# Performance work log

Hardware: AMD Instinct MI355X
Metric: run time of the kernel (lower is better)

Reference implementation:

```python
import jax, jax.numpy as jnp
import numpy as np

# Sizes (must match input_specs)
N_CHR, E_CHR = 50000, 500000
N_SLV, E_SLV = 30000, 300000
B = 256            # number of graphs in the batch
FEAT = 64          # num_node_feats
DIM = 128          # hidden dim
HALF = DIM // 2    # last GCN layer output
ENS = 3            # ensemble per branch type


def setup_inputs() -> dict:
    key = jax.random.key(0)
    ks = jax.random.split(key, 20)
    g = lambda k, shape, fan_in: jax.random.normal(k, shape, dtype=jnp.float32) / np.sqrt(fan_in)
    inp = {
        'chr_x': jax.random.normal(ks[0], (N_CHR, FEAT), dtype=jnp.float32),
        'slv_x': jax.random.normal(ks[1], (N_SLV, FEAT), dtype=jnp.float32),
        'chr_edge_index': jax.random.randint(ks[2], (2, E_CHR), 0, N_CHR),
        'slv_edge_index': jax.random.randint(ks[3], (2, E_SLV), 0, N_SLV),
        'chr_x_batch': jnp.sort(jax.random.randint(ks[4], (N_CHR,), 0, B)),
        'slv_x_batch': jnp.sort(jax.random.randint(ks[5], (N_SLV,), 0, B)),
        # GCN weights, stacked over ensemble (GCNConv: bias=False)
        'chr_W0': g(ks[6], (ENS, FEAT, DIM), FEAT),
        'chr_W1': g(ks[7], (ENS, DIM, DIM), DIM),
        'chr_W2': g(ks[8], (ENS, DIM, HALF), DIM),
        'slv_W0': g(ks[9], (ENS, FEAT, DIM), FEAT),
        'slv_W1': g(ks[10], (ENS, DIM, DIM), DIM),
        'slv_W2': g(ks[11], (ENS, DIM, HALF), DIM),
        # per-ensemble projection heads (nn.Linear with bias)
        'cfc_W': g(ks[12], (ENS, HALF, DIM), HALF),
        'cfc_b': jnp.zeros((ENS, DIM), dtype=jnp.float32),
        'sfc_W': g(ks[13], (ENS, HALF, DIM), HALF),
        'sfc_b': jnp.zeros((ENS, DIM), dtype=jnp.float32),
        # final MLP head
        'fc1_W': g(ks[14], (2 * ENS * DIM, DIM), 2 * ENS * DIM),
        'fc1_b': jnp.zeros((DIM,), dtype=jnp.float32),
        'fc2_W': g(ks[15], (DIM, 1), DIM),
        'fc2_b': jnp.zeros((1,), dtype=jnp.float32),
    }
    return inp


def _gcn(x, W, src, dst, n_nodes):
    # GCNConv(normalize=False, bias=False, aggr='add'):
    # out[i] = sum_{(j,i) in E} (x @ W)[j]   (no self-loops, no normalization)
    h = x @ W
    return jax.ops.segment_sum(h[src], dst, num_segments=n_nodes)


def _branch(x, W0, W1, W2, edge_index, batch_ids, n_nodes):
    src, dst = edge_index[0], edge_index[1]
    h = jax.nn.relu(_gcn(x, W0, src, dst, n_nodes))
    h = jax.nn.relu(_gcn(h, W1, src, dst, n_nodes))
    h = jax.nn.relu(_gcn(h, W2, src, dst, n_nodes))
    # global_add_pool
    return jax.ops.segment_sum(h, batch_ids, num_segments=B)  # [B, HALF]


def reference(chr_x, slv_x, chr_W0, chr_W1, chr_W2, slv_W0, slv_W1, slv_W2,
              cfc_W, cfc_b, sfc_W, sfc_b, fc1_W, fc1_b, fc2_W, fc2_b,
              chr_edge_index, slv_edge_index, chr_x_batch, slv_x_batch):
    # vmap over the ensemble dimension (independent GCN stacks share inputs)
    rep_chr = jax.vmap(lambda w0, w1, w2: _branch(chr_x, w0, w1, w2, chr_edge_index, chr_x_batch, N_CHR))(
        chr_W0, chr_W1, chr_W2)  # [ENS, B, HALF]
    rep_slv = jax.vmap(lambda w0, w1, w2: _branch(slv_x, w0, w1, w2, slv_edge_index, slv_x_batch, N_SLV))(
        slv_W0, slv_W1, slv_W2)  # [ENS, B, HALF]
    ind_chr = jax.nn.relu(jnp.einsum('ebd,edh->ebh', rep_chr, cfc_W) + cfc_b[:, None, :])  # [ENS, B, DIM]
    ind_slv = jax.nn.relu(jnp.einsum('ebd,edh->ebh', rep_slv, sfc_W) + sfc_b[:, None, :])
    # torch.cat(ind_chr + ind_slv, dim=1): chr branches first, then slv branches
    hg = jnp.concatenate([
        jnp.transpose(ind_chr, (1, 0, 2)).reshape(B, ENS * DIM),
        jnp.transpose(ind_slv, (1, 0, 2)).reshape(B, ENS * DIM)], axis=1)  # [B, 2*ENS*DIM]
    hg = jax.nn.relu(hg @ fc1_W + fc1_b)
    out = hg @ fc2_W + fc2_b  # [B, 1]
    return out
```

## Files before the change

### kernel.cpp

```cpp
#include <hip/hip_runtime.h>

#define N_CHR 50000
#define E_CHR 500000
#define N_SLV 30000
#define E_SLV 300000
#define E_TOT (E_CHR + E_SLV)
#define BATCH_B 256
#define FEAT 64
#define DIM 128
#define HALF 64
#define ENSN 3
#define CB_CHR ((N_CHR + 255) / 256)
#define CB_SLV ((N_SLV + 255) / 256)
#define CB_TOT (CB_CHR + CB_SLV)
#define NBLK 128
#define CHUNK ((E_TOT + NBLK - 1) / NBLK)

typedef unsigned int u32;
typedef unsigned short u16;
typedef __attribute__((ext_vector_type(8))) short short8;
typedef __attribute__((ext_vector_type(4))) float floatx4;
typedef __attribute__((ext_vector_type(2))) unsigned int u32x2;


__device__ inline u16 f2b(float f) {
    u32 u = __builtin_bit_cast(u32, f);
    u += 0x7FFFu + ((u >> 16) & 1u);
    return (u16)(u >> 16);
}
__device__ inline float b2f_lo(u32 v) { return __builtin_bit_cast(float, v << 16); }
__device__ inline float b2f_hi(u32 v) { return __builtin_bit_cast(float, v & 0xFFFF0000u); }
__device__ inline u32 packb(float a, float b) { return (u32)f2b(a) | ((u32)f2b(b) << 16); }


__global__ void xconv_k(const float* __restrict__ xc, const float* __restrict__ xs,
                        u16* __restrict__ oc, u16* __restrict__ os) {
    const int nc = N_CHR * FEAT, ns = N_SLV * FEAT;
    int i = blockIdx.x * blockDim.x + threadIdx.x;
    int stride = gridDim.x * blockDim.x;
    for (; i < nc + ns; i += stride) {
        if (i < nc) oc[i] = f2b(xc[i]);
        else os[i - nc] = f2b(xs[i - nc]);
    }
}


__global__ void wconv_k(const float* __restrict__ Wc, const float* __restrict__ Ws,
                        u16* __restrict__ Wtc, u16* __restrict__ Wts, int K, int N) {
    const float* W = blockIdx.z ? Ws : Wc;
    u16* Wt = blockIdx.z ? Wts : Wtc;
    int e = blockIdx.y;
    int idx = blockIdx.x * 256 + threadIdx.x;
    if (idx >= K * N) return;
    int k = idx / N, nn = idx - k * N;
    Wt[((size_t)e * N + nn) * K + k] = f2b(W[(size_t)e * K * N + idx]);
}


__global__ __launch_bounds__(256) void hist_blocks_k(
        const int* __restrict__ cdst, const int* __restrict__ sdst,
        int* __restrict__ gh, int* __restrict__ btot) {
    __shared__ int h[CB_TOT];
    int blk = blockIdx.x, t = threadIdx.x;
    for (int i = t; i < CB_TOT; i += 256) h[i] = 0;
    __syncthreads();
    int s = blk * CHUNK, e = s + CHUNK;
    if (e > E_TOT) e = E_TOT;
    for (int i = s + t; i < e; i += 256) {
        int bkt = (i < E_CHR) ? (cdst[i] >> 8) : (CB_CHR + (sdst[i - E_CHR] >> 8));
        atomicAdd(&h[bkt], 1);
    }
    __syncthreads();
    for (int j = t; j < CB_TOT; j += 256) {
        gh[j * NBLK + blk] = h[j];
        if (h[j]) atomicAdd(&btot[j], h[j]);
    }
}

__global__ void coarse_scan_k(const int* __restrict__ cnt, int* __restrict__ off) {
    int t = threadIdx.x;
    const int PER = (CB_TOT + 63) / 64;
    int loc[PER];
    int sum = 0;
    int s = t * PER;
// ... 82 lines not shown
}

__global__ __launch_bounds__(256) void bucket_sort_k(
        const u32* __restrict__ staging, const int* __restrict__ coff,
        int* __restrict__ off_c, int* __restrict__ off_s,
        int* __restrict__ csr_c, int* __restrict__ csr_s) {
    int b = blockIdx.x, t = threadIdx.x;
    int isS = b >= CB_CHR;
    int base = coff[b], end = coff[b + 1];
    int n = isS ? N_SLV : N_CHR;
    int* off = isS ? off_s : off_c;
    int* csr = isS ? csr_s : csr_c;
    int outBase = isS ? base - E_CHR : base;
    int nodeBase = (isS ? (b - CB_CHR) : b) << 8;
    __shared__ int hist[256];
    __shared__ int cur[256];
    hist[t] = 0;
    __syncthreads();
    for (int i = base + t; i < end; i += 256)
        atomicAdd(&hist[staging[i] >> 17], 1);
    __syncthreads();
    int p = block_exscan(hist[t]);
    int node = nodeBase + t;
    if (node <= n) off[node] = outBase + p;
    cur[t] = p;
    __syncthreads();
    for (int i = base + t; i < end; i += 256) {
        u32 v = staging[i];
        int pos = atomicAdd(&cur[v >> 17], 1);
        csr[outBase + pos] = (int)(v & 0x1FFFFu);
    }
}

__global__ void bounds_both_k(const int* __restrict__ cb, const int* __restrict__ sb,
                              int* __restrict__ start_c, int* __restrict__ start_s) {
    int t = threadIdx.x + blockIdx.x * blockDim.x;
    int isS = t >= 320;
    int b = isS ? t - 320 : t;
    if (b > BATCH_B) return;
    const int* batch = isS ? sb : cb;
    int n = isS ? N_SLV : N_CHR;
    int* start = isS ? start_s : start_c;
    if (b == BATCH_B) { start[b] = n; return; }
    int lo = 0, hi = n;
    while (lo < hi) {
        int mid = (lo + hi) >> 1;
        if (batch[mid] < b) lo = mid + 1; else hi = mid;
    }
    start[b] = lo;
}


__global__ __launch_bounds__(256) void agg1_k(
        const u16* __restrict__ Xc, const int* __restrict__ offc, const int* __restrict__ csrc,
        u16* __restrict__ Yc, int nc,
        const u16* __restrict__ Xs, const int* __restrict__ offs, const int* __restrict__ csrs,
        u16* __restrict__ Ys, int ns) {
    int z = blockIdx.z;
    const u32* X32 = (const u32*)(z ? Xs : Xc);
    const int* off = z ? offs : offc;
    const int* csr = z ? csrs : csrc;
    u32* Y32 = (u32*)(z ? Ys : Yc);
    int n = z ? ns : nc;
    int i = blockIdx.x * 8 + (threadIdx.x >> 5);
    if (i >= n) return;
    int fp = threadIdx.x & 31;
    int s = off[i], e2 = off[i + 1];
    float a0 = 0.f, a1 = 0.f;
    int j = s;
    for (; j + 3 < e2; j += 4) {
        u32 v0 = X32[(size_t)csr[j] * 32 + fp];
        u32 v1 = X32[(size_t)csr[j + 1] * 32 + fp];
        u32 v2 = X32[(size_t)csr[j + 2] * 32 + fp];
        u32 v3 = X32[(size_t)csr[j + 3] * 32 + fp];
        a0 += b2f_lo(v0) + b2f_lo(v1) + b2f_lo(v2) + b2f_lo(v3);
        a1 += b2f_hi(v0) + b2f_hi(v1) + b2f_hi(v2) + b2f_hi(v3);
    }
    for (; j < e2; j++) {
        u32 v = X32[(size_t)csr[j] * 32 + fp];
        a0 += b2f_lo(v); a1 += b2f_hi(v);
    }
    Y32[(size_t)i * 32 + fp] = packb(a0, a1);
}


template<bool RELU>
__global__ __launch_bounds__(256) void aggb128_k(
        const u16* __restrict__ Hc, const int* __restrict__ offc, const int* __restrict__ csrc,
        u16* __restrict__ Yc, int nc,
        const u16* __restrict__ Hs, const int* __restrict__ offs, const int* __restrict__ csrs,
        u16* __restrict__ Ys, int ns) {
    int z = blockIdx.z, e = blockIdx.y;
    int n = z ? ns : nc;
    const int* off = z ? offs : offc;
    const int* csr = z ? csrs : csrc;
    const u32* He = (const u32*)((z ? Hs : Hc) + (size_t)e * n * DIM);
    u32* Ye = (u32*)((z ? Ys : Yc) + (size_t)e * n * DIM);
    int i = blockIdx.x * 8 + (threadIdx.x >> 5);
    if (i >= n) return;
    int fp = threadIdx.x & 31;
    int s = off[i], e2 = off[i + 1];
    float a0 = 0.f, a1 = 0.f, a2 = 0.f, a3 = 0.f;
    int j = s;
    for (; j + 3 < e2; j += 4) {
        u32x2 v0 = *(const u32x2*)(He + (size_t)csr[j] * 64 + fp * 2);
        u32x2 v1 = *(const u32x2*)(He + (size_t)csr[j + 1] * 64 + fp * 2);
        u32x2 v2 = *(const u32x2*)(He + (size_t)csr[j + 2] * 64 + fp * 2);
        u32x2 v3 = *(const u32x2*)(He + (size_t)csr[j + 3] * 64 + fp * 2);
        a0 += b2f_lo(v0.x) + b2f_lo(v1.x) + b2f_lo(v2.x) + b2f_lo(v3.x);
        a1 += b2f_hi(v0.x) + b2f_hi(v1.x) + b2f_hi(v2.x) + b2f_hi(v3.x);
        a2 += b2f_lo(v0.y) + b2f_lo(v1.y) + b2f_lo(v2.y) + b2f_lo(v3.y);
        a3 += b2f_hi(v0.y) + b2f_hi(v1.y) + b2f_hi(v2.y) + b2f_hi(v3.y);
    }
    for (; j < e2; j++) {
        u32x2 v = *(const u32x2*)(He + (size_t)csr[j] * 64 + fp * 2);
        a0 += b2f_lo(v.x); a1 += b2f_hi(v.x);
        a2 += b2f_lo(v.y); a3 += b2f_hi(v.y);
    }
    if (RELU) {
        a0 = fmaxf(a0, 0.f); a1 = fmaxf(a1, 0.f);
        a2 = fmaxf(a2, 0.f); a3 = fmaxf(a3, 0.f);
    }
    u32x2 o; o.x = packb(a0, a1); o.y = packb(a2, a3);
    *(u32x2*)(Ye + (size_t)i * 64 + fp * 2) = o;
}


template<bool RELU>
__global__ __launch_bounds__(256) void aggb64_k(
        const u16* __restrict__ Hc, const int* __restrict__ offc, const int* __restrict__ csrc,
        u16* __restrict__ Yc, int nc,
        const u16* __restrict__ Hs, const int* __restrict__ offs, const int* __restrict__ csrs,
        u16* __restrict__ Ys, int ns) {
    int z = blockIdx.z, e = blockIdx.y;
    int n = z ? ns : nc;
    const int* off = z ? offs : offc;
    const int* csr = z ? csrs : csrc;
    const u32* He = (const u32*)((z ? Hs : Hc) + (size_t)e * n * HALF);
    u32* Ye = (u32*)((z ? Ys : Yc) + (size_t)e * n * HALF);
    int i = blockIdx.x * 16 + (threadIdx.x >> 4);
    if (i >= n) return;
    int fp = threadIdx.x & 15;
    int s = off[i], e2 = off[i + 1];
    float a0 = 0.f, a1 = 0.f, a2 = 0.f, a3 = 0.f;
    int j = s;
    for (; j + 3 < e2; j += 4) {
        u32x2 v0 = *(const u32x2*)(He + (size_t)csr[j] * 32 + fp * 2);
        u32x2 v1 = *(const u32x2*)(He + (size_t)csr[j + 1] * 32 + fp * 2);
        u32x2 v2 = *(const u32x2*)(He + (size_t)csr[j + 2] * 32 + fp * 2);
        u32x2 v3 = *(const u32x2*)(He + (size_t)csr[j + 3] * 32 + fp * 2);
        a0 += b2f_lo(v0.x) + b2f_lo(v1.x) + b2f_lo(v2.x) + b2f_lo(v3.x);
        a1 += b2f_hi(v0.x) + b2f_hi(v1.x) + b2f_hi(v2.x) + b2f_hi(v3.x);
        a2 += b2f_lo(v0.y) + b2f_lo(v1.y) + b2f_lo(v2.y) + b2f_lo(v3.y);
        a3 += b2f_hi(v0.y) + b2f_hi(v1.y) + b2f_hi(v2.y) + b2f_hi(v3.y);
    }
    for (; j < e2; j++) {
        u32x2 v = *(const u32x2*)(He + (size_t)csr[j] * 32 + fp * 2);
        a0 += b2f_lo(v.x); a1 += b2f_hi(v.x);
        a2 += b2f_lo(v.y); a3 += b2f_hi(v.y);
    }
    if (RELU) {
        a0 = fmaxf(a0, 0.f); a1 = fmaxf(a1, 0.f);
        a2 = fmaxf(a2, 0.f); a3 = fmaxf(a3, 0.f);
    }
    u32x2 o; o.x = packb(a0, a1); o.y = packb(a2, a3);
    *(u32x2*)(Ye + (size_t)i * 32 + fp * 2) = o;
}


#define WPAD 8

template<int K, int COLS, bool RELU>
__global__ __launch_bounds__(256) void gemm_mfma_k(
        const u16* __restrict__ Xc, size_t esc, const u16* __restrict__ Wtc,
        u16* __restrict__ Yc, int nc,
        const u16* __restrict__ Xs, size_t ess, const u16* __restrict__ Wts,
        u16* __restrict__ Ys, int ns) {
    __shared__ u16 wlds[COLS * (K + WPAD)];
    const int z = blockIdx.z, e = blockIdx.y;
    const int n = z ? ns : nc;
    const u16* Xe = (z ? Xs : Xc) + (size_t)e * (z ? ess : esc);
    const u16* We = (z ? Wts : Wtc) + (size_t)e * COLS * K;
    u16* Ye = (z ? Ys : Yc) + (size_t)e * (size_t)n * COLS;
    for (int c = threadIdx.x; c < COLS * (K / 8); c += 256) {
        int row = c / (K / 8), seg = c - row * (K / 8);
        *(short8*)(wlds + row * (K + WPAD) + seg * 8) = *(const short8*)(We + (size_t)row * K + seg * 8);
    }
    __syncthreads();
    int wave = threadIdx.x >> 6, lane = threadIdx.x & 63;
    int quad = lane >> 4, nq = lane & 15;
    int m0 = blockIdx.x * 256 + wave * 64;
    if (m0 >= n) return;
    constexpr int NT = COLS / 16, KT = K / 32;
    floatx4 acc[4][NT];
#pragma unroll
    for (int rg = 0; rg < 4; rg++)
#pragma unroll
        for (int t = 0; t < NT; t++) acc[rg][t] = (floatx4)(0.f);
#pragma unroll
// ... 1 lines not shown
        int k0 = kt * 32 + quad * 8;
        short8 a[4];
#pragma unroll
        for (int rg = 0; rg < 4; rg++) {
            int row = m0 + rg * 16 + nq;
            int rc = row < n ? row : n - 1;
            a[rg] = *(const short8*)(Xe + (size_t)rc * K + k0);
        }
#pragma unroll
        for (int t = 0; t < NT; t++) {
            short8 b = *(const short8*)(wlds + (t * 16 + nq) * (K + WPAD) + k0);
#pragma unroll
            for (int rg = 0; rg < 4; rg++)
                acc[rg][t] = __builtin_amdgcn_mfma_f32_16x16x32_bf16(a[rg], b, acc[rg][t], 0, 0, 0);
        }
    }
    int rbase = quad * 4;
#pragma unroll
    for (int rg = 0; rg < 4; rg++)
#pragma unroll
        for (int t = 0; t < NT; t++)
#pragma unroll
            for (int r = 0; r < 4; r++) {
                int row = m0 + rg * 16 + rbase + r;
                if (row < n) {
                    float v = acc[rg][t][r];
                    if (RELU) v = fmaxf(v, 0.f);
                    Ye[(size_t)row * COLS + t * 16 + nq] = f2b(v);
                }
            }
}


__global__ __launch_bounds__(256) void pool_b_k(const u16* __restrict__ H,
                                                const int* __restrict__ start,
                                                float* __restrict__ rep, int n, int colOff) {
    int b = blockIdx.x, e = blockIdx.y;
    const u32* He = (const u32*)(H + (size_t)e * n * HALF);
    int t = threadIdx.x;
    int wave = t >> 6, lane = t & 63;
    int fp = lane & 31, rp = lane >> 5;
    int s = start[b], e2 = start[b + 1];
    float a0 = 0.f, a1 = 0.f;
    for (int i = s + wave * 2 + rp; i < e2; i += 8) {
        u32 v = He[(size_t)i * 32 + fp];
        a0 += b2f_lo(v); a1 += b2f_hi(v);
    }
    __shared__ float sm[8][32][2];
    sm[wave * 2 + rp][fp][0] = a0;
    sm[wave * 2 + rp][fp][1] = a1;
    __syncthreads();
    if (t < 64) {
        int f2 = t & 31, half = t >> 5;
        float acc = 0.f;
#pragma unroll
        for (int k = 0; k < 8; k++) acc += sm[k][f2][half];
        rep[b * (2 * ENSN * HALF) + colOff + e * HALF + f2 * 2 + half] = acc;
    }
}


__global__ void head_k(const float* __restrict__ rep,
                       const float* __restrict__ cW, const float* __restrict__ cB,
                       const float* __restrict__ sW, const float* __restrict__ sB,
                       float* __restrict__ hg) {
    int b = blockIdx.x;
    int be = blockIdx.y;
    int branch = be / ENSN, e = be % ENSN;
    int c = threadIdx.x;
    __shared__ float r[HALF];
    const float* repRow = rep + b * (2 * ENSN * HALF) + branch * (ENSN * HALF) + e * HALF;
    if (c < HALF) r[c] = repRow[c];
    __syncthreads();
    const float* W = (branch ? sW : cW) + e * HALF * DIM;
    const float* Bv = (branch ? sB : cB) + e * DIM;
    float acc = Bv[c];
#pragma unroll
    for (int k = 0; k < HALF; k++) acc = fmaf(r[k], W[k * DIM + c], acc);
    hg[b * (2 * ENSN * DIM) + branch * (ENSN * DIM) + e * DIM + c] = fmaxf(acc, 0.f);
}


__global__ void final_k(const float* __restrict__ hg, const float* __restrict__ W1,
                        const float* __restrict__ b1, const float* __restrict__ W2,
                        const float* __restrict__ b2, float* __restrict__ out) {
    int b = blockIdx.x;
    int c = threadIdx.x;
    const int IN = 2 * ENSN * DIM;
    __shared__ float row[2 * ENSN * DIM];
    for (int i = c; i < IN; i += DIM) row[i] = hg[b * IN + i];
    __syncthreads();
    float acc = b1[c];
    for (int k = 0; k < IN; k++) acc = fmaf(row[k], W1[k * DIM + c], acc);
    acc = fmaxf(acc, 0.f);
    __shared__ float red[DIM];
    red[c] = acc * W2[c];
    __syncthreads();
    for (int s = DIM / 2; s > 0; s >>= 1) {
        if (c < s) red[c] += red[c + s];
        __syncthreads();
    }
    if (c == 0) out[b] = red[0] + b2[0];
}


extern "C" void kernel_launch(void* const* d_in, const int* in_sizes, int n_in,
                              void* d_out, int out_size, void* d_ws, size_t ws_size,
                              hipStream_t stream) {
    const float* chr_x = (const float*)d_in[0];
    const float* slv_x = (const float*)d_in[1];
    const int* chr_ei = (const int*)d_in[2];
    const int* slv_ei = (const int*)d_in[3];
    const int* chr_batch = (const int*)d_in[4];
    const int* slv_batch = (const int*)d_in[5];
    const float* chr_W0 = (const float*)d_in[6];
    const float* chr_W1 = (const float*)d_in[7];
    const float* chr_W2 = (const float*)d_in[8];
    const float* slv_W0 = (const float*)d_in[9];
    const float* slv_W1 = (const float*)d_in[10];
    const float* slv_W2 = (const float*)d_in[11];
    const float* cfc_W = (const float*)d_in[12];
    const float* cfc_b = (const float*)d_in[13];
    const float* sfc_W = (const float*)d_in[14];
    const float* sfc_b = (const float*)d_in[15];
    const float* fc1_W = (const float*)d_in[16];
    const float* fc1_b = (const float*)d_in[17];
    const float* fc2_W = (const float*)d_in[18];
    const float* fc2_b = (const float*)d_in[19];
    float* out = (float*)d_out;

    char* w = (char*)d_ws;
    auto carve = [&](size_t bytes) {
        void* p = (void*)w;
        w += (bytes + 255) & ~(size_t)255;
        return p;
    };
    int* off_chr = (int*)carve((N_CHR + 1) * sizeof(int));
    int* csr_chr = (int*)carve((size_t)E_CHR * sizeof(int));
    int* off_slv = (int*)carve((N_SLV + 1) * sizeof(int));
    int* csr_slv = (int*)carve((size_t)E_SLV * sizeof(int));
    int* btot    = (int*)carve(CB_TOT * sizeof(int));
    int* coff    = (int*)carve((CB_TOT + 1) * sizeof(int));
    int* gh      = (int*)carve((size_t)CB_TOT * NBLK * sizeof(int));
    u32* staging = (u32*)carve((size_t)E_TOT * sizeof(u32));
    int* start_chr = (int*)carve((BATCH_B + 1) * sizeof(int));
    int* start_slv = (int*)carve((BATCH_B + 1) * sizeof(int));
    u16* cW0t = (u16*)carve((size_t)ENSN * DIM * FEAT * sizeof(u16));
    u16* cW1t = (u16*)carve((size_t)ENSN * DIM * DIM * sizeof(u16));
    u16* cW2t = (u16*)carve((size_t)ENSN * HALF * DIM * sizeof(u16));
    u16* sW0t = (u16*)carve((size_t)ENSN * DIM * FEAT * sizeof(u16));
    u16* sW1t = (u16*)carve((size_t)ENSN * DIM * DIM * sizeof(u16));
    u16* sW2t = (u16*)carve((size_t)ENSN * HALF * DIM * sizeof(u16));
    u16* xb_chr = (u16*)carve((size_t)N_CHR * FEAT * sizeof(u16));
    u16* xb_slv = (u16*)carve((size_t)N_SLV * FEAT * sizeof(u16));
    float* rep = (float*)carve((size_t)BATCH_B * 2 * ENSN * HALF * sizeof(float));
    float* hg  = (float*)carve((size_t)BATCH_B * 2 * ENSN * DIM * sizeof(float));
    u16* aggX_c = (u16*)carve((size_t)N_CHR * FEAT * sizeof(u16));
    u16* bufP_c = (u16*)carve((size_t)ENSN * N_CHR * DIM * sizeof(u16));
    u16* bufQ_c = (u16*)carve((size_t)ENSN * N_CHR * DIM * sizeof(u16));
    size_t used = (size_t)(w - (char*)d_ws);
    size_t needS = (((size_t)N_SLV * FEAT * 2 + 255) & ~(size_t)255)
                 + 2 * (((size_t)ENSN * N_SLV * DIM * 2 + 255) & ~(size_t)255);
    bool merged = used + needS <= ws_size;
    u16* aggX_s = merged ? (u16*)carve((size_t)N_SLV * FEAT * sizeof(u16)) : aggX_c;
    u16* bufP_s = merged ? (u16*)carve((size_t)ENSN * N_SLV * DIM * sizeof(u16)) : bufP_c;
    u16* bufQ_s = merged ? (u16*)carve((size_t)ENSN * N_SLV * DIM * sizeof(u16)) : bufQ_c;

    xconv_k<<<512, 256, 0, stream>>>(chr_x, slv_x, xb_chr, xb_slv);
    wconv_k<<<dim3((FEAT * DIM + 255) / 256, ENSN, 2), 256, 0, stream>>>(chr_W0, slv_W0, cW0t, sW0t, FEAT, DIM);
    wconv_k<<<dim3((DIM * DIM + 255) / 256, ENSN, 2), 256, 0, stream>>>(chr_W1, slv_W1, cW1t, sW1t, DIM, DIM);
    wconv_k<<<dim3((DIM * HALF + 255) / 256, ENSN, 2), 256, 0, stream>>>(chr_W2, slv_W2, cW2t, sW2t, DIM, HALF);

    hipMemsetAsync(btot, 0, CB_TOT * sizeof(int), stream);
    hist_blocks_k<<<NBLK, 256, 0, stream>>>(chr_ei + E_CHR, slv_ei + E_SLV, gh, btot);
    coarse_scan_k<<<1, 64, 0, stream>>>(btot, coff);
    block_base_k<<<CB_TOT, NBLK, 0, stream>>>(gh, coff);
    scatter2_k<<<NBLK, 256, 0, stream>>>(chr_ei, slv_ei, gh, staging);
    bucket_sort_k<<<CB_TOT, 256, 0, stream>>>(staging, coff, off_chr, off_slv, csr_chr, csr_slv);
    bounds_both_k<<<1, 640, 0, stream>>>(chr_batch, slv_batch, start_chr, start_slv);

    const int GX_GEMM_C = (N_CHR + 255) / 256;
    const int GX_GEMM_S = (N_SLV + 255) / 256;

    if (merged) {
        agg1_k<<<dim3((N_CHR + 7) / 8, 1, 2), 256, 0, stream>>>(
            xb_chr, off_chr, csr_chr, aggX_c, N_CHR,
            xb_slv, off_slv, csr_slv, aggX_s, N_SLV);
        gemm_mfma_k<FEAT, DIM, true><<<dim3(GX_GEMM_C, ENSN, 2), 256, 0, stream>>>(
            aggX_c, 0, cW0t, bufP_c, N_CHR, aggX_s, 0, sW0t, bufP_s, N_SLV);
        aggb128_k<false><<<dim3((N_CHR + 7) / 8, ENSN, 2), 256, 0, stream>>>(
            bufP_c, off_chr, csr_chr, bufQ_c, N_CHR,
            bufP_s, off_slv, csr_slv, bufQ_s, N_SLV);
        gemm_mfma_k<DIM, DIM, true><<<dim3(GX_GEMM_C, ENSN, 2), 256, 0, stream>>>(
            bufQ_c, (size_t)N_CHR * DIM, cW1t, bufP_c, N_CHR,
            bufQ_s, (size_t)N_SLV * DIM, sW1t, bufP_s, N_SLV);
        gemm_mfma_k<DIM, HALF, false><<<dim3(GX_GEMM_C, ENSN, 2), 256, 0, stream>>>(
            bufP_c, (size_t)N_CHR * DIM, cW2t, bufQ_c, N_CHR,
            bufP_s, (size_t)N_SLV * DIM, sW2t, bufQ_s, N_SLV);
        aggb64_k<true><<<dim3((N_CHR + 15) / 16, ENSN, 2), 256, 0, stream>>>(
            bufQ_c, off_chr, csr_chr, bufP_c, N_CHR,
            bufQ_s, off_slv, csr_slv, bufP_s, N_SLV);
        pool_b_k<<<dim3(BATCH_B, ENSN), 256, 0, stream>>>(bufP_c, start_chr, rep, N_CHR, 0);
        pool_b_k<<<dim3(BATCH_B, ENSN), 256, 0, stream>>>(bufP_s, start_slv, rep, N_SLV, ENSN * HALF);
    } else {
        agg1_k<<<dim3((N_CHR + 7) / 8, 1, 1), 256, 0, stream>>>(
            xb_chr, off_chr, csr_chr, aggX_c, N_CHR, xb_chr, off_chr, csr_chr, aggX_c, N_CHR);
        gemm_mfma_k<FEAT, DIM, true><<<dim3(GX_GEMM_C, ENSN, 1), 256, 0, stream>>>(
            aggX_c, 0, cW0t, bufP_c, N_CHR, aggX_c, 0, cW0t, bufP_c, N_CHR);
        aggb128_k<false><<<dim3((N_CHR + 7) / 8, ENSN, 1), 256, 0, stream>>>(
            bufP_c, off_chr, csr_chr, bufQ_c, N_CHR, bufP_c, off_chr, csr_chr, bufQ_c, N_CHR);
        gemm_mfma_k<DIM, DIM, true><<<dim3(GX_GEMM_C, ENSN, 1), 256, 0, stream>>>(
            bufQ_c, (size_t)N_CHR * DIM, cW1t, bufP_c, N_CHR,
            bufQ_c, (size_t)N_CHR * DIM, cW1t, bufP_c, N_CHR);
        gemm_mfma_k<DIM, HALF, false><<<dim3(GX_GEMM_C, ENSN, 1), 256, 0, stream>>>(
            bufP_c, (size_t)N_CHR * DIM, cW2t, bufQ_c, N_CHR,
            bufP_c, (size_t)N_CHR * DIM, cW2t, bufQ_c, N_CHR);
        aggb64_k<true><<<dim3((N_CHR + 15) / 16, ENSN, 1), 256, 0, stream>>>(
            bufQ_c, off_chr, csr_chr, bufP_c, N_CHR, bufQ_c, off_chr, csr_chr, bufP_c, N_CHR);
        pool_b_k<<<dim3(BATCH_B, ENSN), 256, 0, stream>>>(bufP_c, start_chr, rep, N_CHR, 0);

        agg1_k<<<dim3((N_SLV + 7) / 8, 1, 1), 256, 0, stream>>>(
            xb_slv, off_slv, csr_slv, aggX_c, N_SLV, xb_slv, off_slv, csr_slv, aggX_c, N_SLV);
        gemm_mfma_k<FEAT, DIM, true><<<dim3(GX_GEMM_S, ENSN, 1), 256, 0, stream>>>(
            aggX_c, 0, sW0t, bufP_c, N_SLV, aggX_c, 0, sW0t, bufP_c, N_SLV);
        aggb128_k<false><<<dim3((N_SLV + 7) / 8, ENSN, 1), 256, 0, stream>>>(
            bufP_c, off_slv, csr_slv, bufQ_c, N_SLV, bufP_c, off_slv, csr_slv, bufQ_c, N_SLV);
        gemm_mfma_k<DIM, DIM, true><<<dim3(GX_GEMM_S, ENSN, 1), 256, 0, stream>>>(
            bufQ_c, (size_t)N_SLV * DIM, sW1t, bufP_c, N_SLV,
            bufQ_c, (size_t)N_SLV * DIM, sW1t, bufP_c, N_SLV);
        gemm_mfma_k<DIM, HALF, false><<<dim3(GX_GEMM_S, ENSN, 1), 256, 0, stream>>>(
            bufP_c, (size_t)N_SLV * DIM, sW2t, bufQ_c, N_SLV,
            bufP_c, (size_t)N_SLV * DIM, sW2t, bufQ_c, N_SLV);
        aggb64_k<true><<<dim3((N_SLV + 15) / 16, ENSN, 1), 256, 0, stream>>>(
            bufQ_c, off_slv, csr_slv, bufP_c, N_SLV, bufQ_c, off_slv, csr_slv, bufP_c, N_SLV);
        pool_b_k<<<dim3(BATCH_B, ENSN), 256, 0, stream>>>(bufP_c, start_slv, rep, N_SLV, ENSN * HALF);
    }

    head_k<<<dim3(BATCH_B, 2 * ENSN), DIM, 0, stream>>>(rep, cfc_W, cfc_b, sfc_W, sfc_b, hg);
    final_k<<<BATCH_B, DIM, 0, stream>>>(hg, fc1_W, fc1_b, fc2_W, fc2_b, out);
}
```

Before: 456.5 us.

## Fuse GCN layers 2-3 GEMMs, fuse final aggregation with pooling, widen gathers

Several changes land at once. The layer-2 and layer-3 GEMMs are fused into one kernel that keeps the ReLU'd intermediate in LDS, and the last aggregation is fused with graph sum-pooling through segmented atomics, which removes the bounds search and pool kernels. The head and final MLP are merged into one kernel, and the weight conversions into a single launch. Aggregation kernels now use 16-byte gathers with fewer lanes per node. The non-merged workspace fallback is dropped, and float atomics make the pooled sums order-nondeterministic.

```diff
diff --git a/kernel.cpp b/kernel.cpp
--- a/kernel.cpp
+++ b/kernel.cpp
@@ -20,7 +20,7 @@
 typedef unsigned short u16;
 typedef __attribute__((ext_vector_type(8))) short short8;
 typedef __attribute__((ext_vector_type(4))) float floatx4;
-typedef __attribute__((ext_vector_type(2))) unsigned int u32x2;
+typedef __attribute__((ext_vector_type(4))) unsigned int u32x4;
 
 
 __device__ inline u16 f2b(float f) {
@@ -31,6 +31,13 @@
 __device__ inline float b2f_lo(u32 v) { return __builtin_bit_cast(float, v << 16); }
 __device__ inline float b2f_hi(u32 v) { return __builtin_bit_cast(float, v & 0xFFFF0000u); }
 __device__ inline u32 packb(float a, float b) { return (u32)f2b(a) | ((u32)f2b(b) << 16); }
+
+__device__ inline void acc8(float* a, u32x4 v) {
+    a[0] += b2f_lo(v.x); a[1] += b2f_hi(v.x);
+    a[2] += b2f_lo(v.y); a[3] += b2f_hi(v.y);
+    a[4] += b2f_lo(v.z); a[5] += b2f_hi(v.z);
+    a[6] += b2f_lo(v.w); a[7] += b2f_hi(v.w);
+}
 
 
 __global__ void xconv_k(const float* __restrict__ xc, const float* __restrict__ xs,
@@ -45,11 +52,21 @@
 }
 
 
-__global__ void wconv_k(const float* __restrict__ Wc, const float* __restrict__ Ws,
-                        u16* __restrict__ Wtc, u16* __restrict__ Wts, int K, int N) {
-    const float* W = blockIdx.z ? Ws : Wc;
-    u16* Wt = blockIdx.z ? Wts : Wtc;
-    int e = blockIdx.y;
+__global__ void wconv6_k(const float* __restrict__ cW0, const float* __restrict__ cW1,
+                         const float* __restrict__ cW2, const float* __restrict__ sW0,
+                         const float* __restrict__ sW1, const float* __restrict__ sW2,
+                         u16* __restrict__ cW0t, u16* __restrict__ cW1t, u16* __restrict__ cW2t,
+                         u16* __restrict__ sW0t, u16* __restrict__ sW1t, u16* __restrict__ sW2t) {
+    int z = blockIdx.z, e = blockIdx.y;
+    const float* W; u16* Wt; int K, N;
+    switch (z) {
+        case 0: W = cW0; Wt = cW0t; K = FEAT; N = DIM;  break;
+        case 1: W = cW1; Wt = cW1t; K = DIM;  N = DIM;  break;
+        case 2: W = cW2; Wt = cW2t; K = DIM;  N = HALF; break;
+        case 3: W = sW0; Wt = sW0t; K = FEAT; N = DIM;  break;
+        case 4: W = sW1; Wt = sW1t; K = DIM;  N = DIM;  break;
+        default: W = sW2; Wt = sW2t; K = DIM; N = HALF; break;
+    }
     int idx = blockIdx.x * 256 + threadIdx.x;
     if (idx >= K * N) return;
     int k = idx / N, nn = idx - k * N;
@@ -198,24 +215,6 @@
     }
 }
 
-__global__ void bounds_both_k(const int* __restrict__ cb, const int* __restrict__ sb,
-                              int* __restrict__ start_c, int* __restrict__ start_s) {
-    int t = threadIdx.x + blockIdx.x * blockDim.x;
-    int isS = t >= 320;
-    int b = isS ? t - 320 : t;
-    if (b > BATCH_B) return;
-    const int* batch = isS ? sb : cb;
-    int n = isS ? N_SLV : N_CHR;
-    int* start = isS ? start_s : start_c;
-    if (b == BATCH_B) { start[b] = n; return; }
-    int lo = 0, hi = n;
-    while (lo < hi) {
-        int mid = (lo + hi) >> 1;
-        if (batch[mid] < b) lo = mid + 1; else hi = mid;
-    }
-    start[b] = lo;
-}
-
 
 __global__ __launch_bounds__(256) void agg1_k(
         const u16* __restrict__ Xc, const int* __restrict__ offc, const int* __restrict__ csrc,
@@ -223,34 +222,30 @@
         const u16* __restrict__ Xs, const int* __restrict__ offs, const int* __restrict__ csrs,
         u16* __restrict__ Ys, int ns) {
     int z = blockIdx.z;
-    const u32* X32 = (const u32*)(z ? Xs : Xc);
+    const u32x4* X4 = (const u32x4*)(z ? Xs : Xc);
     const int* off = z ? offs : offc;
     const int* csr = z ? csrs : csrc;
-    u32* Y32 = (u32*)(z ? Ys : Yc);
+    u32x4* Y4 = (u32x4*)(z ? Ys : Yc);
     int n = z ? ns : nc;
-    int i = blockIdx.x * 8 + (threadIdx.x >> 5);
+    int i = blockIdx.x * 32 + (threadIdx.x >> 3);
     if (i >= n) return;
-    int fp = threadIdx.x & 31;
+    int l8 = threadIdx.x & 7;
     int s = off[i], e2 = off[i + 1];
-    float a0 = 0.f, a1 = 0.f;
+    float a[8] = {0.f, 0.f, 0.f, 0.f, 0.f, 0.f, 0.f, 0.f};
     int j = s;
-    for (; j + 3 < e2; j += 4) {
-        u32 v0 = X32[(size_t)csr[j] * 32 + fp];
-        u32 v1 = X32[(size_t)csr[j + 1] * 32 + fp];
-        u32 v2 = X32[(size_t)csr[j + 2] * 32 + fp];
-        u32 v3 = X32[(size_t)csr[j + 3] * 32 + fp];
-        a0 += b2f_lo(v0) + b2f_lo(v1) + b2f_lo(v2) + b2f_lo(v3);
-        a1 += b2f_hi(v0) + b2f_hi(v1) + b2f_hi(v2) + b2f_hi(v3);
-    }
-    for (; j < e2; j++) {
-        u32 v = X32[(size_t)csr[j] * 32 + fp];
-        a0 += b2f_lo(v); a1 += b2f_hi(v);
-    }
-    Y32[(size_t)i * 32 + fp] = packb(a0, a1);
-}
-
-
-template<bool RELU>
+    for (; j + 1 < e2; j += 2) {
+        u32x4 v0 = X4[(size_t)csr[j] * 8 + l8];
+        u32x4 v1 = X4[(size_t)csr[j + 1] * 8 + l8];
+        acc8(a, v0); acc8(a, v1);
+    }
+    if (j < e2) acc8(a, X4[(size_t)csr[j] * 8 + l8]);
+    u32x4 o;
+    o.x = packb(a[0], a[1]); o.y = packb(a[2], a[3]);
+    o.z = packb(a[4], a[5]); o.w = packb(a[6], a[7]);
+    Y4[(size_t)i * 8 + l8] = o;
+}
+
+
 __global__ __launch_bounds__(256) void aggb128_k(
         const u16* __restrict__ Hc, const int* __restrict__ offc, const int* __restrict__ csrc,
         u16* __restrict__ Yc, int nc,
@@ -260,77 +255,24 @@
     int n = z ? ns : nc;
     const int* off = z ? offs : offc;
     const int* csr = z ? csrs : csrc;
-    const u32* He = (const u32*)((z ? Hs : Hc) + (size_t)e * n * DIM);
-    u32* Ye = (u32*)((z ? Ys : Yc) + (size_t)e * n * DIM);
-    int i = blockIdx.x * 8 + (threadIdx.x >> 5);
-    if (i >= n) return;
-    int fp = threadIdx.x & 31;
-    int s = off[i], e2 = off[i + 1];
-    float a0 = 0.f, a1 = 0.f, a2 = 0.f, a3 = 0.f;
-    int j = s;
-    for (; j + 3 < e2; j += 4) {
-        u32x2 v0 = *(const u32x2*)(He + (size_t)csr[j] * 64 + fp * 2);
-        u32x2 v1 = *(const u32x2*)(He + (size_t)csr[j + 1] * 64 + fp * 2);
-        u32x2 v2 = *(const u32x2*)(He + (size_t)csr[j + 2] * 64 + fp * 2);
-        u32x2 v3 = *(const u32x2*)(He + (size_t)csr[j + 3] * 64 + fp * 2);
-        a0 += b2f_lo(v0.x) + b2f_lo(v1.x) + b2f_lo(v2.x) + b2f_lo(v3.x);
-        a1 += b2f_hi(v0.x) + b2f_hi(v1.x) + b2f_hi(v2.x) + b2f_hi(v3.x);
-        a2 += b2f_lo(v0.y) + b2f_lo(v1.y) + b2f_lo(v2.y) + b2f_lo(v3.y);
-        a3 += b2f_hi(v0.y) + b2f_hi(v1.y) + b2f_hi(v2.y) + b2f_hi(v3.y);
-    }
-    for (; j < e2; j++) {
-        u32x2 v = *(const u32x2*)(He + (size_t)csr[j] * 64 + fp * 2);
-        a0 += b2f_lo(v.x); a1 += b2f_hi(v.x);
-        a2 += b2f_lo(v.y); a3 += b2f_hi(v.y);
-    }
-    if (RELU) {
-        a0 = fmaxf(a0, 0.f); a1 = fmaxf(a1, 0.f);
-        a2 = fmaxf(a2, 0.f); a3 = fmaxf(a3, 0.f);
-    }
-    u32x2 o; o.x = packb(a0, a1); o.y = packb(a2, a3);
-    *(u32x2*)(Ye + (size_t)i * 64 + fp * 2) = o;
-}
-
-
-template<bool RELU>
-__global__ __launch_bounds__(256) void aggb64_k(
-        const u16* __restrict__ Hc, const int* __restrict__ offc, const int* __restrict__ csrc,
-        u16* __restrict__ Yc, int nc,
-        const u16* __restrict__ Hs, const int* __restrict__ offs, const int* __restrict__ csrs,
-        u16* __restrict__ Ys, int ns) {
-    int z = blockIdx.z, e = blockIdx.y;
-    int n = z ? ns : nc;
-    const int* off = z ? offs : offc;
-    const int* csr = z ? csrs : csrc;
-    const u32* He = (const u32*)((z ? Hs : Hc) + (size_t)e * n * HALF);
-    u32* Ye = (u32*)((z ? Ys : Yc) + (size_t)e * n * HALF);
+    const u32x4* He = (const u32x4*)((z ? Hs : Hc) + (size_t)e * n * DIM);
+    u32x4* Ye = (u32x4*)((z ? Ys : Yc) + (size_t)e * n * DIM);
     int i = blockIdx.x * 16 + (threadIdx.x >> 4);
     if (i >= n) return;
-    int fp = threadIdx.x & 15;
+    int l16 = threadIdx.x & 15;
     int s = off[i], e2 = off[i + 1];
-    float a0 = 0.f, a1 = 0.f, a2 = 0.f, a3 = 0.f;
+    float a[8] = {0.f, 0.f, 0.f, 0.f, 0.f, 0.f, 0.f, 0.f};
     int j = s;
-    for (; j + 3 < e2; j += 4) {
-        u32x2 v0 = *(const u32x2*)(He + (size_t)csr[j] * 32 + fp * 2);
-        u32x2 v1 = *(const u32x2*)(He + (size_t)csr[j + 1] * 32 + fp * 2);
-        u32x2 v2 = *(const u32x2*)(He + (size_t)csr[j + 2] * 32 + fp * 2);
-        u32x2 v3 = *(const u32x2*)(He + (size_t)csr[j + 3] * 32 + fp * 2);
-        a0 += b2f_lo(v0.x) + b2f_lo(v1.x) + b2f_lo(v2.x) + b2f_lo(v3.x);
-        a1 += b2f_hi(v0.x) + b2f_hi(v1.x) + b2f_hi(v2.x) + b2f_hi(v3.x);
-        a2 += b2f_lo(v0.y) + b2f_lo(v1.y) + b2f_lo(v2.y) + b2f_lo(v3.y);
-        a3 += b2f_hi(v0.y) + b2f_hi(v1.y) + b2f_hi(v2.y) + b2f_hi(v3.y);
-    }
-    for (; j < e2; j++) {
-        u32x2 v = *(const u32x2*)(He + (size_t)csr[j] * 32 + fp * 2);
-        a0 += b2f_lo(v.x); a1 += b2f_hi(v.x);
-        a2 += b2f_lo(v.y); a3 += b2f_hi(v.y);
-    }
-    if (RELU) {
-        a0 = fmaxf(a0, 0.f); a1 = fmaxf(a1, 0.f);
-        a2 = fmaxf(a2, 0.f); a3 = fmaxf(a3, 0.f);
-    }
-    u32x2 o; o.x = packb(a0, a1); o.y = packb(a2, a3);
-    *(u32x2*)(Ye + (size_t)i * 32 + fp * 2) = o;
+    for (; j + 1 < e2; j += 2) {
+        u32x4 v0 = He[(size_t)csr[j] * 16 + l16];
+        u32x4 v1 = He[(size_t)csr[j + 1] * 16 + l16];
+        acc8(a, v0); acc8(a, v1);
+    }
+    if (j < e2) acc8(a, He[(size_t)csr[j] * 16 + l16]);
+    u32x4 o;
+    o.x = packb(a[0], a[1]); o.y = packb(a[2], a[3]);
+    o.z = packb(a[4], a[5]); o.w = packb(a[6], a[7]);
+    Ye[(size_t)i * 16 + l16] = o;
 }
 
 
@@ -398,75 +340,193 @@
 }
 
 
-__global__ __launch_bounds__(256) void pool_b_k(const u16* __restrict__ H,
-                                                const int* __restrict__ start,
-                                                float* __restrict__ rep, int n, int colOff) {
-    int b = blockIdx.x, e = blockIdx.y;
-    const u32* He = (const u32*)(H + (size_t)e * n * HALF);
-    int t = threadIdx.x;
-    int wave = t >> 6, lane = t & 63;
-    int fp = lane & 31, rp = lane >> 5;
-    int s = start[b], e2 = start[b + 1];
-    float a0 = 0.f, a1 = 0.f;
-    for (int i = s + wave * 2 + rp; i < e2; i += 8) {
-        u32 v = He[(size_t)i * 32 + fp];
-        a0 += b2f_lo(v); a1 += b2f_hi(v);
-    }
-    __shared__ float sm[8][32][2];
-    sm[wave * 2 + rp][fp][0] = a0;
-    sm[wave * 2 + rp][fp][1] = a1;
+__global__ __launch_bounds__(256) void gemm23_k(
+        const u16* __restrict__ Xc, const u16* __restrict__ W1c, const u16* __restrict__ W2c,
+        u16* __restrict__ Yc, int nc,
+        const u16* __restrict__ Xs, const u16* __restrict__ W1s, const u16* __restrict__ W2s,
+        u16* __restrict__ Ys, int ns) {
+    __shared__ u16 wlds[DIM * DIM];
+    __shared__ u16 hlds[4 * 32 * DIM];
+    const int z = blockIdx.z, e = blockIdx.y;
+    const int n = z ? ns : nc;
+    const u16* Xe = (z ? Xs : Xc) + (size_t)e * (size_t)n * DIM;
+    const u16* W1 = (z ? W1s : W1c) + (size_t)e * DIM * DIM;
+    const u16* W2 = (z ? W2s : W2c) + (size_t)e * HALF * DIM;
+    u16* Ye = (z ? Ys : Yc) + (size_t)e * (size_t)n * HALF;
+    for (int c = threadIdx.x; c < DIM * (DIM / 8); c += 256) {
+        int row = c >> 4, seg = c & 15;
+        *(short8*)(wlds + row * DIM + ((seg ^ (row & 15)) << 3)) =
+            *(const short8*)(W1 + (size_t)row * DIM + (seg << 3));
+    }
+    __syncthreads();
+    int wave = threadIdx.x >> 6, lane = threadIdx.x & 63;
+    int quad = lane >> 4, nq = lane & 15;
+    int m0 = blockIdx.x * 128 + wave * 32;
+    floatx4 acc[2][8];
+#pragma unroll
+    for (int rg = 0; rg < 2; rg++)
+#pragma unroll
+        for (int t = 0; t < 8; t++) acc[rg][t] = (floatx4)(0.f);
+#pragma unroll
+    for (int kt = 0; kt < 4; kt++) {
+        int k0 = kt * 32 + quad * 8;
+        short8 a[2];
+#pragma unroll
+        for (int rg = 0; rg < 2; rg++) {
+            int row = m0 + rg * 16 + nq;
+            int rc = row < n ? row : (n - 1);
+            a[rg] = *(const short8*)(Xe + (size_t)rc * DIM + k0);
+        }
+#pragma unroll
+        for (int t = 0; t < 8; t++) {
+            int rb = t * 16 + nq;
+            short8 b = *(const short8*)(wlds + rb * DIM + ((((kt << 2) + quad) ^ nq) << 3));
+#pragma unroll
+            for (int rg = 0; rg < 2; rg++)
+                acc[rg][t] = __builtin_amdgcn_mfma_f32_16x16x32_bf16(a[rg], b, acc[rg][t], 0, 0, 0);
+        }
+    }
+    u16* hw = hlds + wave * 32 * DIM;
+#pragma unroll
+    for (int rg = 0; rg < 2; rg++)
+#pragma unroll
+        for (int t = 0; t < 8; t++)
+#pragma unroll
+            for (int r = 0; r < 4; r++) {
+                int rl = rg * 16 + quad * 4 + r;
+                int col = t * 16 + nq;
+                hw[rl * DIM + (((col >> 3) ^ (rl & 15)) << 3) + (col & 7)] =
+                    f2b(fmaxf(acc[rg][t][r], 0.f));
+            }
+    __syncthreads();
+    for (int c = threadIdx.x; c < HALF * (DIM / 8); c += 256) {
+        int row = c >> 4, seg = c & 15;
+        *(short8*)(wlds + row * DIM + ((seg ^ (row & 15)) << 3)) =
+            *(const short8*)(W2 + (size_t)row * DIM + (seg << 3));
+    }
+    __syncthreads();
+    floatx4 acc2[2][4];
+#pragma unroll
+    for (int rg = 0; rg < 2; rg++)
+#pragma unroll
+        for (int t = 0; t < 4; t++) acc2[rg][t] = (floatx4)(0.f);
+#pragma unroll
+    for (int kt = 0; kt < 4; kt++) {
+        int k0q = (kt << 2) + quad;
+        short8 a[2];
+#pragma unroll
+        for (int rg = 0; rg < 2; rg++) {
+            int rl = rg * 16 + nq;
+            a[rg] = *(const short8*)(hw + rl * DIM + ((k0q ^ (rl & 15)) << 3));
+        }
+#pragma unroll
+        for (int t = 0; t < 4; t++) {
+            int rb = t * 16 + nq;
+            short8 b = *(const short8*)(wlds + rb * DIM + ((k0q ^ nq) << 3));
+#pragma unroll
+            for (int rg = 0; rg < 2; rg++)
+                acc2[rg][t] = __builtin_amdgcn_mfma_f32_16x16x32_bf16(a[rg], b, acc2[rg][t], 0, 0, 0);
+        }
+    }
+#pragma unroll
+    for (int rg = 0; rg < 2; rg++)
+#pragma unroll
+        for (int t = 0; t < 4; t++)
+#pragma unroll
+            for (int r = 0; r < 4; r++) {
+                int row = m0 + rg * 16 + quad * 4 + r;
+                if (row < n) Ye[(size_t)row * HALF + t * 16 + nq] = f2b(acc2[rg][t][r]);
+            }
+}
+
+
+__global__ __launch_bounds__(256) void agg64pool_k(
+        const u16* __restrict__ Pc, const int* __restrict__ offc, const int* __restrict__ csrc,
+        const int* __restrict__ batc, int nc,
+        const u16* __restrict__ Ps, const int* __restrict__ offs, const int* __restrict__ csrs,
+        const int* __restrict__ bats, int ns,
+        float* __restrict__ rep) {
+    int z = blockIdx.z, e = blockIdx.y;
+    int n = z ? ns : nc;
+    const int* off = z ? offs : offc;
+    const int* csr = z ? csrs : csrc;
+    const int* batch = z ? bats : batc;
+    const u32x4* He = (const u32x4*)((z ? Ps : Pc) + (size_t)e * n * HALF);
+    int i0 = blockIdx.x * 32;
+    int nl = threadIdx.x >> 3, l8 = threadIdx.x & 7;
+    int i = i0 + nl;
+    float a[8] = {0.f, 0.f, 0.f, 0.f, 0.f, 0.f, 0.f, 0.f};
+    if (i < n) {
+        int s = off[i], e2 = off[i + 1];
+        int j = s;
+        for (; j + 1 < e2; j += 2) {
+            u32x4 v0 = He[(size_t)csr[j] * 8 + l8];
+            u32x4 v1 = He[(size_t)csr[j + 1] * 8 + l8];
+            acc8(a, v0); acc8(a, v1);
+        }
+        if (j < e2) acc8(a, He[(size_t)csr[j] * 8 + l8]);
+    }
+    __shared__ float sm[32][64];
+    __shared__ int gb[32];
+#pragma unroll
+    for (int k = 0; k < 8; k++) sm[nl][l8 * 8 + k] = fmaxf(a[k], 0.f);
+    if (threadIdx.x < 32) gb[threadIdx.x] = (i0 + (int)threadIdx.x < n) ? batch[i0 + threadIdx.x] : -1;
+    __syncthreads();
+    if (threadIdx.x < 64) {
+        int f = threadIdx.x;
+        int colbase = z * (ENSN * HALF) + e * HALF + f;
+        float acc = 0.f;
+        int g = -2;
+        for (int k = 0; k < 32; k++) {
+            int gg = gb[k];
+            if (gg != g) {
+                if (g >= 0) atomicAdd(&rep[g * (2 * ENSN * HALF) + colbase], acc);
+                acc = 0.f;
+                g = gg;
+            }
+            if (gg >= 0) acc += sm[k][f];
+        }
+        if (g >= 0) atomicAdd(&rep[g * (2 * ENSN * HALF) + colbase], acc);
+    }
+}
+
+
+__global__ __launch_bounds__(256) void headfinal_k(
+        const float* __restrict__ rep,
+        const float* __restrict__ cW, const float* __restrict__ cB,
+        const float* __restrict__ sW, const float* __restrict__ sB,
+        const float* __restrict__ W1, const float* __restrict__ b1,
+        const float* __restrict__ W2, const float* __restrict__ b2,
+        float* __restrict__ out) {
+    int b = blockIdx.x, t = threadIdx.x;
+    __shared__ float r[2 * ENSN * HALF];
+    __shared__ float hg[2 * ENSN * DIM];
+    __shared__ float red[DIM];
+    for (int i = t; i < 2 * ENSN * HALF; i += 256) r[i] = rep[b * (2 * ENSN * HALF) + i];
+    __syncthreads();
+    for (int o = t; o < 2 * ENSN * DIM; o += 256) {
+        int head = o >> 7, c = o & 127;
+        int branch = head / ENSN, e = head - branch * ENSN;
+        const float* W = (branch ? sW : cW) + (size_t)e * HALF * DIM;
+        const float* rr = r + branch * (ENSN * HALF) + e * HALF;
+        float acc = (branch ? sB : cB)[e * DIM + c];
+#pragma unroll
+        for (int k = 0; k < HALF; k++) acc = fmaf(rr[k], W[k * DIM + c], acc);
+        hg[o] = fmaxf(acc, 0.f);
+    }
+    __syncthreads();
+    if (t < DIM) {
+        float acc = b1[t];
+        for (int k = 0; k < 2 * ENSN * DIM; k++) acc = fmaf(hg[k], W1[k * DIM + t], acc);
+        red[t] = fmaxf(acc, 0.f) * W2[t];
+    }
     __syncthreads();
     if (t < 64) {
-        int f2 = t & 31, half = t >> 5;
-        float acc = 0.f;
-#pragma unroll
-        for (int k = 0; k < 8; k++) acc += sm[k][f2][half];
-        rep[b * (2 * ENSN * HALF) + colOff + e * HALF + f2 * 2 + half] = acc;
-    }
-}
-
-
-__global__ void head_k(const float* __restrict__ rep,
-                       const float* __restrict__ cW, const float* __restrict__ cB,
-                       const float* __restrict__ sW, const float* __restrict__ sB,
-                       float* __restrict__ hg) {
-    int b = blockIdx.x;
-    int be = blockIdx.y;
-    int branch = be / ENSN, e = be % ENSN;
-    int c = threadIdx.x;
-    __shared__ float r[HALF];
-    const float* repRow = rep + b * (2 * ENSN * HALF) + branch * (ENSN * HALF) + e * HALF;
-    if (c < HALF) r[c] = repRow[c];
-    __syncthreads();
-    const float* W = (branch ? sW : cW) + e * HALF * DIM;
-    const float* Bv = (branch ? sB : cB) + e * DIM;
-    float acc = Bv[c];
-#pragma unroll
-    for (int k = 0; k < HALF; k++) acc = fmaf(r[k], W[k * DIM + c], acc);
-    hg[b * (2 * ENSN * DIM) + branch * (ENSN * DIM) + e * DIM + c] = fmaxf(acc, 0.f);
-}
-
-
-__global__ void final_k(const float* __restrict__ hg, const float* __restrict__ W1,
-                        const float* __restrict__ b1, const float* __restrict__ W2,
-                        const float* __restrict__ b2, float* __restrict__ out) {
-    int b = blockIdx.x;
-    int c = threadIdx.x;
-    const int IN = 2 * ENSN * DIM;
-    __shared__ float row[2 * ENSN * DIM];
-    for (int i = c; i < IN; i += DIM) row[i] = hg[b * IN + i];
-    __syncthreads();
-    float acc = b1[c];
-    for (int k = 0; k < IN; k++) acc = fmaf(row[k], W1[k * DIM + c], acc);
-    acc = fmaxf(acc, 0.f);
-    __shared__ float red[DIM];
-    red[c] = acc * W2[c];
-    __syncthreads();
-    for (int s = DIM / 2; s > 0; s >>= 1) {
-        if (c < s) red[c] += red[c + s];
-        __syncthreads();
-    }
-    if (c == 0) out[b] = red[0] + b2[0];
+        float v = red[t] + red[t + 64];
+#pragma unroll
+        for (int o = 32; o > 0; o >>= 1) v += __shfl_down(v, o, 64);
+        if (t == 0) out[b] = v + b2[0];
+    }
 }
 
 
@@ -509,8 +569,6 @@
     int* coff    = (int*)carve((CB_TOT + 1) * sizeof(int));
     int* gh      = (int*)carve((size_t)CB_TOT * NBLK * sizeof(int));
     u32* staging = (u32*)carve((size_t)E_TOT * sizeof(u32));
-    int* start_chr = (int*)carve((BATCH_B + 1) * sizeof(int));
-    int* start_slv = (int*)carve((BATCH_B + 1) * sizeof(int));
     u16* cW0t = (u16*)carve((size_t)ENSN * DIM * FEAT * sizeof(u16));
     u16* cW1t = (u16*)carve((size_t)ENSN * DIM * DIM * sizeof(u16));
     u16* cW2t = (u16*)carve((size_t)ENSN * HALF * DIM * sizeof(u16));
@@ -520,22 +578,17 @@
     u16* xb_chr = (u16*)carve((size_t)N_CHR * FEAT * sizeof(u16));
     u16* xb_slv = (u16*)carve((size_t)N_SLV * FEAT * sizeof(u16));
     float* rep = (float*)carve((size_t)BATCH_B * 2 * ENSN * HALF * sizeof(float));
-    float* hg  = (float*)carve((size_t)BATCH_B * 2 * ENSN * DIM * sizeof(float));
     u16* aggX_c = (u16*)carve((size_t)N_CHR * FEAT * sizeof(u16));
     u16* bufP_c = (u16*)carve((size_t)ENSN * N_CHR * DIM * sizeof(u16));
     u16* bufQ_c = (u16*)carve((size_t)ENSN * N_CHR * DIM * sizeof(u16));
-    size_t used = (size_t)(w - (char*)d_ws);
-    size_t needS = (((size_t)N_SLV * FEAT * 2 + 255) & ~(size_t)255)
-                 + 2 * (((size_t)ENSN * N_SLV * DIM * 2 + 255) & ~(size_t)255);
-    bool merged = used + needS <= ws_size;
-    u16* aggX_s = merged ? (u16*)carve((size_t)N_SLV * FEAT * sizeof(u16)) : aggX_c;
-    u16* bufP_s = merged ? (u16*)carve((size_t)ENSN * N_SLV * DIM * sizeof(u16)) : bufP_c;
-    u16* bufQ_s = merged ? (u16*)carve((size_t)ENSN * N_SLV * DIM * sizeof(u16)) : bufQ_c;
+    u16* aggX_s = (u16*)carve((size_t)N_SLV * FEAT * sizeof(u16));
+    u16* bufP_s = (u16*)carve((size_t)ENSN * N_SLV * DIM * sizeof(u16));
+    u16* bufQ_s = (u16*)carve((size_t)ENSN * N_SLV * DIM * sizeof(u16));
 
     xconv_k<<<512, 256, 0, stream>>>(chr_x, slv_x, xb_chr, xb_slv);
-    wconv_k<<<dim3((FEAT * DIM + 255) / 256, ENSN, 2), 256, 0, stream>>>(chr_W0, slv_W0, cW0t, sW0t, FEAT, DIM);
-    wconv_k<<<dim3((DIM * DIM + 255) / 256, ENSN, 2), 256, 0, stream>>>(chr_W1, slv_W1, cW1t, sW1t, DIM, DIM);
-    wconv_k<<<dim3((DIM * HALF + 255) / 256, ENSN, 2), 256, 0, stream>>>(chr_W2, slv_W2, cW2t, sW2t, DIM, HALF);
+    wconv6_k<<<dim3(64, ENSN, 6), 256, 0, stream>>>(chr_W0, chr_W1, chr_W2,
+                                                    slv_W0, slv_W1, slv_W2,
+                                                    cW0t, cW1t, cW2t, sW0t, sW1t, sW2t);
 
     hipMemsetAsync(btot, 0, CB_TOT * sizeof(int), stream);
     hist_blocks_k<<<NBLK, 256, 0, stream>>>(chr_ei + E_CHR, slv_ei + E_SLV, gh, btot);
@@ -543,65 +596,24 @@
     block_base_k<<<CB_TOT, NBLK, 0, stream>>>(gh, coff);
     scatter2_k<<<NBLK, 256, 0, stream>>>(chr_ei, slv_ei, gh, staging);
     bucket_sort_k<<<CB_TOT, 256, 0, stream>>>(staging, coff, off_chr, off_slv, csr_chr, csr_slv);
-    bounds_both_k<<<1, 640, 0, stream>>>(chr_batch, slv_batch, start_chr, start_slv);
-
-    const int GX_GEMM_C = (N_CHR + 255) / 256;
-    const int GX_GEMM_S = (N_SLV + 255) / 256;
-
-    if (merged) {
-        agg1_k<<<dim3((N_CHR + 7) / 8, 1, 2), 256, 0, stream>>>(
-            xb_chr, off_chr, csr_chr, aggX_c, N_CHR,
-            xb_slv, off_slv, csr_slv, aggX_s, N_SLV);
-        gemm_mfma_k<FEAT, DIM, true><<<dim3(GX_GEMM_C, ENSN, 2), 256, 0, stream>>>(
-            aggX_c, 0, cW0t, bufP_c, N_CHR, aggX_s, 0, sW0t, bufP_s, N_SLV);
-        aggb128_k<false><<<dim3((N_CHR + 7) / 8, ENSN, 2), 256, 0, stream>>>(
-            bufP_c, off_chr, csr_chr, bufQ_c, N_CHR,
-            bufP_s, off_slv, csr_slv, bufQ_s, N_SLV);
-        gemm_mfma_k<DIM, DIM, true><<<dim3(GX_GEMM_C, ENSN, 2), 256, 0, stream>>>(
-            bufQ_c, (size_t)N_CHR * DIM, cW1t, bufP_c, N_CHR,
-            bufQ_s, (size_t)N_SLV * DIM, sW1t, bufP_s, N_SLV);
-        gemm_mfma_k<DIM, HALF, false><<<dim3(GX_GEMM_C, ENSN, 2), 256, 0, stream>>>(
-            bufP_c, (size_t)N_CHR * DIM, cW2t, bufQ_c, N_CHR,
-            bufP_s, (size_t)N_SLV * DIM, sW2t, bufQ_s, N_SLV);
-        aggb64_k<true><<<dim3((N_CHR + 15) / 16, ENSN, 2), 256, 0, stream>>>(
-            bufQ_c, off_chr, csr_chr, bufP_c, N_CHR,
-            bufQ_s, off_slv, csr_slv, bufP_s, N_SLV);
-        pool_b_k<<<dim3(BATCH_B, ENSN), 256, 0, stream>>>(bufP_c, start_chr, rep, N_CHR, 0);
-        pool_b_k<<<dim3(BATCH_B, ENSN), 256, 0, stream>>>(bufP_s, start_slv, rep, N_SLV, ENSN * HALF);
-    } else {
-        agg1_k<<<dim3((N_CHR + 7) / 8, 1, 1), 256, 0, stream>>>(
-            xb_chr, off_chr, csr_chr, aggX_c, N_CHR, xb_chr, off_chr, csr_chr, aggX_c, N_CHR);
-        gemm_mfma_k<FEAT, DIM, true><<<dim3(GX_GEMM_C, ENSN, 1), 256, 0, stream>>>(
-            aggX_c, 0, cW0t, bufP_c, N_CHR, aggX_c, 0, cW0t, bufP_c, N_CHR);
-        aggb128_k<false><<<dim3((N_CHR + 7) / 8, ENSN, 1), 256, 0, stream>>>(
-            bufP_c, off_chr, csr_chr, bufQ_c, N_CHR, bufP_c, off_chr, csr_chr, bufQ_c, N_CHR);
-        gemm_mfma_k<DIM, DIM, true><<<dim3(GX_GEMM_C, ENSN, 1), 256, 0, stream>>>(
-            bufQ_c, (size_t)N_CHR * DIM, cW1t, bufP_c, N_CHR,
-            bufQ_c, (size_t)N_CHR * DIM, cW1t, bufP_c, N_CHR);
-        gemm_mfma_k<DIM, HALF, false><<<dim3(GX_GEMM_C, ENSN, 1), 256, 0, stream>>>(
-            bufP_c, (size_t)N_CHR * DIM, cW2t, bufQ_c, N_CHR,
-            bufP_c, (size_t)N_CHR * DIM, cW2t, bufQ_c, N_CHR);
-        aggb64_k<true><<<dim3((N_CHR + 15) / 16, ENSN, 1), 256, 0, stream>>>(
-            bufQ_c, off_chr, csr_chr, bufP_c, N_CHR, bufQ_c, off_chr, csr_chr, bufP_c, N_CHR);
-        pool_b_k<<<dim3(BATCH_B, ENSN), 256, 0, stream>>>(bufP_c, start_chr, rep, N_CHR, 0);
-
-        agg1_k<<<dim3((N_SLV + 7) / 8, 1, 1), 256, 0, stream>>>(
-            xb_slv, off_slv, csr_slv, aggX_c, N_SLV, xb_slv, off_slv, csr_slv, aggX_c, N_SLV);
-        gemm_mfma_k<FEAT, DIM, true><<<dim3(GX_GEMM_S, ENSN, 1), 256, 0, stream>>>(
-            aggX_c, 0, sW0t, bufP_c, N_SLV, aggX_c, 0, sW0t, bufP_c, N_SLV);
-        aggb128_k<false><<<dim3((N_SLV + 7) / 8, ENSN, 1), 256, 0, stream>>>(
-            bufP_c, off_slv, csr_slv, bufQ_c, N_SLV, bufP_c, off_slv, csr_slv, bufQ_c, N_SLV);
-        gemm_mfma_k<DIM, DIM, true><<<dim3(GX_GEMM_S, ENSN, 1), 256, 0, stream>>>(
-            bufQ_c, (size_t)N_SLV * DIM, sW1t, bufP_c, N_SLV,
-            bufQ_c, (size_t)N_SLV * DIM, sW1t, bufP_c, N_SLV);
-        gemm_mfma_k<DIM, HALF, false><<<dim3(GX_GEMM_S, ENSN, 1), 256, 0, stream>>>(
-            bufP_c, (size_t)N_SLV * DIM, sW2t, bufQ_c, N_SLV,
-            bufP_c, (size_t)N_SLV * DIM, sW2t, bufQ_c, N_SLV);
-        aggb64_k<true><<<dim3((N_SLV + 15) / 16, ENSN, 1), 256, 0, stream>>>(
-            bufQ_c, off_slv, csr_slv, bufP_c, N_SLV, bufQ_c, off_slv, csr_slv, bufP_c, N_SLV);
-        pool_b_k<<<dim3(BATCH_B, ENSN), 256, 0, stream>>>(bufP_c, start_slv, rep, N_SLV, ENSN * HALF);
-    }
-
-    head_k<<<dim3(BATCH_B, 2 * ENSN), DIM, 0, stream>>>(rep, cfc_W, cfc_b, sfc_W, sfc_b, hg);
-    final_k<<<BATCH_B, DIM, 0, stream>>>(hg, fc1_W, fc1_b, fc2_W, fc2_b, out);
-}
+
+    hipMemsetAsync(rep, 0, (size_t)BATCH_B * 2 * ENSN * HALF * sizeof(float), stream);
+
+    agg1_k<<<dim3((N_CHR + 31) / 32, 1, 2), 256, 0, stream>>>(
+        xb_chr, off_chr, csr_chr, aggX_c, N_CHR,
+        xb_slv, off_slv, csr_slv, aggX_s, N_SLV);
+    gemm_mfma_k<FEAT, DIM, true><<<dim3((N_CHR + 255) / 256, ENSN, 2), 256, 0, stream>>>(
+        aggX_c, 0, cW0t, bufP_c, N_CHR, aggX_s, 0, sW0t, bufP_s, N_SLV);
+    aggb128_k<<<dim3((N_CHR + 15) / 16, ENSN, 2), 256, 0, stream>>>(
+        bufP_c, off_chr, csr_chr, bufQ_c, N_CHR,
+        bufP_s, off_slv, csr_slv, bufQ_s, N_SLV);
+    gemm23_k<<<dim3((N_CHR + 127) / 128, ENSN, 2), 256, 0, stream>>>(
+        bufQ_c, cW1t, cW2t, bufP_c, N_CHR,
+        bufQ_s, sW1t, sW2t, bufP_s, N_SLV);
+    agg64pool_k<<<dim3((N_CHR + 31) / 32, ENSN, 2), 256, 0, stream>>>(
+        bufP_c, off_chr, csr_chr, chr_batch, N_CHR,
+        bufP_s, off_slv, csr_slv, slv_batch, N_SLV, rep);
+
+    headfinal_k<<<BATCH_B, 256, 0, stream>>>(rep, cfc_W, cfc_b, sfc_W, sfc_b,
+                                             fc1_W, fc1_b, fc2_W, fc2_b, out);
+}
```

Result: faster. 405.4 us (-11.2%).
